# Kernel optimization log

Measured on AMD Instinct MI355X. Metric: run time of the kernel, lower is better.

Reference implementation:

```python
import jax, jax.numpy as jnp
import numpy as np


def _lstm_step(x, h, c, Wih, Whh, bih, bhh):
    # torch.nn.LSTMCell gate order: i, f, g, o
    g = x @ Wih.T + h @ Whh.T + bih + bhh
    i, f, gg, o = jnp.split(g, 4, axis=-1)
    c2 = jax.nn.sigmoid(f) * c + jax.nn.sigmoid(i) * jnp.tanh(gg)
    h2 = jax.nn.sigmoid(o) * jnp.tanh(c2)
    return h2, c2


def _run_dir(x_pad, mask, h0, c0, Wih, Whh, bih, bhh, reverse):
    # Masked scan == VariableRecurrent: rows past batch_sizes[t] keep frozen state.
    def step(carry, inp):
        h, c = carry
        x_t, m = inp
        h2, c2 = _lstm_step(x_t, h, c, Wih, Whh, bih, bhh)
        m = m[:, None]
        h = jnp.where(m, h2, h)
        c = jnp.where(m, c2, c)
        return (h, c), h
    (hT, cT), outs = jax.lax.scan(step, (h0, c0), (x_pad, mask), reverse=reverse)
    return hT, cT, outs


def setup_inputs():
    key = jax.random.key(0)
    B, T, D, CELL, L = 64, 1024, 256, 128, 2
    G = 4 * CELL  # 512
    lengths = np.array([T - 8 * b for b in range(B)])  # 1024 .. 520, descending
    batch_sizes = jnp.asarray([(lengths > t).sum() for t in range(T)], dtype=jnp.int32)
    total = int(lengths.sum())  # 49408
    ks = jax.random.split(key, 5)
    inp = jax.random.normal(ks[0], (total, D), dtype=jnp.float32)
    W_ih = jax.random.normal(ks[1], (2 * L, G, D), jnp.float32) * 0.05
    W_hh = jax.random.normal(ks[2], (2 * L, G, CELL), jnp.float32) * 0.05
    b_ih = jax.random.normal(ks[3], (2 * L, G), jnp.float32) * 0.05
    b_hh = jax.random.normal(ks[4], (2 * L, G), jnp.float32) * 0.05
    h0 = jnp.zeros((2 * L, B, CELL), jnp.float32)
    c0 = jnp.zeros((2 * L, B, CELL), jnp.float32)
    return {"input": inp, "batch_sizes": batch_sizes, "h0": h0, "c0": c0,
            "W_ih": W_ih, "W_hh": W_hh, "b_ih": b_ih, "b_hh": b_hh}


def reference(input, batch_sizes, h0, c0, W_ih, W_hh, b_ih, b_hh):
    T = batch_sizes.shape[0]
    B = h0.shape[1]
    total = input.shape[0]
    num_layers = W_ih.shape[0] // 2
    # packed <-> padded index math (static shapes; values from batch_sizes)
    offsets = jnp.concatenate([jnp.zeros((1,), batch_sizes.dtype),
                               jnp.cumsum(batch_sizes)[:-1]])  # [T]
    bidx = jnp.arange(B)
    mask = bidx[None, :] < batch_sizes[:, None]  # [T, B] valid rows per step
    gather_idx = jnp.clip(offsets[:, None] + bidx[None, :], 0, total - 1)
    x = input[gather_idx]  # padded [T, B, D]; invalid rows masked in scan
    tok = jnp.arange(total)
    t_idx = jnp.searchsorted(offsets, tok, side='right') - 1
    b_idx = tok - offsets[t_idx]
    hs, cs = [], []
    for l in range(num_layers):
        outs = []
        for d in range(2):  # layer ordering: fwd_l, rev_l (matches StackedRNN)
            k = 2 * l + d
            hT, cT, o = _run_dir(x, mask, h0[k], c0[k],
                                 W_ih[k], W_hh[k], b_ih[k], b_hh[k],
                                 reverse=(d == 1))
            hs.append(hT)
            cs.append(cT)
            outs.append(o)
        x = jnp.concatenate(outs, axis=-1)  # [T, B, hidden_size]
    h_n = jnp.stack(hs, 0)  # [total_layers, B, CELL]
    c_n = jnp.stack(cs, 0)
    packed_out = x[t_idx, b_idx]  # [total, hidden_size]
    return packed_out, h_n, c_n
```

## Files before the change

### kernel.cpp

```cpp
#include <hip/hip_runtime.h>
#include <hip/hip_fp16.h>
#include <hip/hip_bf16.h>


#define CELL 128
#define GATES 512
#define DIN 256
#define NB 64

typedef float f4_t __attribute__((ext_vector_type(4)));
typedef short bf8_t __attribute__((ext_vector_type(8)));
typedef _Float16 h2_t __attribute__((ext_vector_type(2)));

static __device__ __forceinline__ unsigned short f32_bf16(float f) {
  union { float f; unsigned int u; } v; v.f = f;
  unsigned int u = v.u;
  return (unsigned short)((u + 0x7fffu + ((u >> 16) & 1u)) >> 16);
}

__global__ void k_setup(const int* __restrict__ bs, int T,
                        int* __restrict__ offsets, int* __restrict__ lengths) {
  __shared__ int sbs[1024];
  int t = threadIdx.x;
  sbs[t] = (t < T) ? bs[t] : 0;
  __syncthreads();
  int sum = 0;
  for (int i = 0; i < t; ++i) sum += sbs[i];
  if (t < T) offsets[t] = sum;
  if (t < NB) {
    int c = 0;
    for (int i = 0; i < T; ++i) c += (sbs[i] > t) ? 1 : 0;
    lengths[t] = c;
  }
}

__global__ void k_convert(const float* __restrict__ x, unsigned short* __restrict__ xb, int nx,
                          const float* __restrict__ wih, unsigned short* __restrict__ wb, int nw,
                          const float* __restrict__ bih, const float* __restrict__ bhh,
                          float* __restrict__ bsum, int nb2) {
  int stride = gridDim.x * blockDim.x;
  int i0 = blockIdx.x * blockDim.x + threadIdx.x;
  for (int i = i0; i < nx; i += stride) xb[i] = f32_bf16(x[i]);
  for (int i = i0; i < nw; i += stride) wb[i] = f32_bf16(wih[i]);
  for (int i = i0; i < nb2; i += stride) bsum[i] = bih[i] + bhh[i];
}

__global__ __launch_bounds__(256) void k_gemm(
    const unsigned short* __restrict__ A,
    const unsigned short* __restrict__ W,
    const float* __restrict__ bsum,
    __half* __restrict__ C,
    int M, int lbase) {
  __shared__ __align__(16) unsigned short As[128 * 64];
  __shared__ __align__(16) unsigned short Bs[128 * 64];
  const int tid = threadIdx.x;
  const int lane = tid & 63;
  const int wave = tid >> 6;
  const int wm = wave >> 1, wn = wave & 1;
  const int m0 = blockIdx.x * 128;
  const int n0 = blockIdx.y * 128;

  f4_t acc[4][4];
#pragma unroll
  for (int i = 0; i < 4; ++i)
#pragma unroll
    for (int j = 0; j < 4; ++j) acc[i][j] = (f4_t){0.f, 0.f, 0.f, 0.f};

  for (int kt = 0; kt < 256; kt += 64) {
#pragma unroll
    for (int it = 0; it < 4; ++it) {
      int idx = it * 256 + tid;
      int row = idx >> 3;
      int gslot = (idx & 7) ^ (row & 7);
      int grow = m0 + row; if (grow > M - 1) grow = M - 1;
      __builtin_amdgcn_global_load_lds(
          (const __attribute__((address_space(1))) unsigned int*)(A + (size_t)grow * 256 + kt + gslot * 8),
          (__attribute__((address_space(3))) unsigned int*)(As + idx * 8), 16, 0, 0);
    }
#pragma unroll
    for (int it = 0; it < 4; ++it) {
      int idx = it * 256 + tid;
      int row = idx >> 3;
      int gslot = (idx & 7) ^ (row & 7);
      __builtin_amdgcn_global_load_lds(
          (const __attribute__((address_space(1))) unsigned int*)(W + (size_t)(lbase + n0 + row) * 256 + kt + gslot * 8),
          (__attribute__((address_space(3))) unsigned int*)(Bs + idx * 8), 16, 0, 0);
    }
    asm volatile("s_waitcnt vmcnt(0)" ::: "memory");
    __syncthreads();
#pragma unroll
    for (int kk = 0; kk < 2; ++kk) {
      bf8_t af[4], bfv[4];
#pragma unroll
      for (int i = 0; i < 4; ++i) {
        int arow = wm * 64 + i * 16 + (lane & 15);
        int aslot = (kk * 4 + (lane >> 4)) ^ (arow & 7);
        af[i] = *(const bf8_t*)(As + arow * 64 + aslot * 8);
        int brow = wn * 64 + i * 16 + (lane & 15);
        int bslot = (kk * 4 + (lane >> 4)) ^ (brow & 7);
        bfv[i] = *(const bf8_t*)(Bs + brow * 64 + bslot * 8);
      }
#pragma unroll
      for (int i = 0; i < 4; ++i)
#pragma unroll
        for (int j = 0; j < 4; ++j)
          acc[i][j] = __builtin_amdgcn_mfma_f32_16x16x32_bf16(af[i], bfv[j], acc[i][j], 0, 0, 0);
    }
    __syncthreads();
  }
#pragma unroll
  for (int i = 0; i < 4; ++i) {
#pragma unroll
    for (int j = 0; j < 4; ++j) {
      int col = n0 + wn * 64 + j * 16 + (lane & 15);
      float bv = bsum[lbase + col];
#pragma unroll
      for (int r = 0; r < 4; ++r) {
        int row = m0 + wm * 64 + i * 16 + (lane >> 4) * 4 + r;
        if (row < M) C[(size_t)row * 1024 + col] = (__half)(acc[i][j][r] + bv);
      }
    }
  }
}

#if defined(__has_builtin)
#if __has_builtin(__builtin_amdgcn_fdot2)
#define HAVE_FDOT2 1
#endif
#endif

static __device__ __forceinline__ float fdot2(h2_t a, h2_t b, float c) {
#ifdef HAVE_FDOT2
  return __builtin_amdgcn_fdot2(a, b, c, false);
#else
  return c + (float)a[0] * (float)b[0] + (float)a[1] * (float)b[1];
#endif
}
static __device__ __forceinline__ float sigm(float x) { return 1.f / (1.f + __expf(-x)); }
static __device__ __forceinline__ float tanh_(float x) { return 1.f - 2.f / (1.f + __expf(2.f * x)); }

static __device__ __forceinline__ float red16(float v) {
  return v + __int_as_float(__builtin_amdgcn_ds_swizzle(__float_as_int(v), 0x401F));
}
static __device__ __forceinline__ float red32(float v) {
  return v + __shfl_xor(v, 32, 64);
}

template <int LAYER>
__global__ __launch_bounds__(512) void k_rec(
    const __half* __restrict__ gates,
    const int* __restrict__ offsets,
    const int* __restrict__ lengths,
    const float* __restrict__ h0,
    const float* __restrict__ c0,
    const float* __restrict__ Whh,
    unsigned short* __restrict__ y1,
    float* __restrict__ outp,
    float* __restrict__ hn, float* __restrict__ cn,
    int T) {
  const int b = blockIdx.x >> 1;
  const int d = blockIdx.x & 1;
  const int k = 2 * LAYER + d;
  const int tid = threadIdx.x;
  const int lane = tid & 63;
  const int wave = tid >> 6;
  const int q = wave * 16 + (lane & 15);
  const int s = lane >> 4;
  const int L = lengths[b];

  __shared__ __align__(16) __half hb[2][CELL];
  __shared__ int toks[1024];

  for (int t = tid; t < T; t += 512) toks[t] = offsets[t] + b;

  h2_t wp[4][16];
  {
    const float* Wb = Whh + (size_t)k * GATES * CELL;
#pragma unroll
    for (int gi = 0; gi < 4; ++gi) {
      const float2* rowp = (const float2*)(Wb + (size_t)(gi * CELL + q) * CELL + s * 32);
#pragma unroll
      for (int j = 0; j < 16; ++j) {
        float2 w = rowp[j];
        h2_t p; p[0] = (_Float16)w.x; p[1] = (_Float16)w.y;
        wp[gi][j] = p;
      }
    }
  }

  float hcur = h0[(size_t)k * NB * CELL + b * CELL + q];
  float ccur = c0[(size_t)k * NB * CELL + b * CELL + q];
  if (s == 0) hb[0][q] = (__half)hcur;
  __syncthreads();

  __half gx0 = __half(0.f), gx1 = __half(0.f), gx2 = __half(0.f), gx3 = __half(0.f);
  int tokc = 0;
  if (L > 0) {
    tokc = toks[d ? (L - 1) : 0];
    const __half* gp = gates + (size_t)tokc * 1024 + d * GATES + q;
    gx0 = gp[0]; gx1 = gp[CELL]; gx2 = gp[2 * CELL]; gx3 = gp[3 * CELL];
  }

  int p = 0;
  for (int n = 0; n < L; ++n) {
    int tokn = tokc;
    if (n + 1 < L) tokn = toks[d ? (L - 2 - n) : (n + 1)];
    __half gn0, gn1, gn2, gn3;
    {
      const __half* gp = gates + (size_t)tokn * 1024 + d * GATES + q;
      gn0 = gp[0]; gn1 = gp[CELL]; gn2 = gp[2 * CELL]; gn3 = gp[3 * CELL];
    }

    const h2_t* hsh = (const h2_t*)hb[p];
    h2_t hp[16];
#pragma unroll
    for (int j = 0; j < 16; ++j) hp[j] = hsh[s * 16 + j];
    float a0 = 0.f, a1 = 0.f, a2 = 0.f, a3 = 0.f;
#pragma unroll
    for (int j = 0; j < 16; ++j) {
      a0 = fdot2(wp[0][j], hp[j], a0);
      a1 = fdot2(wp[1][j], hp[j], a1);
      a2 = fdot2(wp[2][j], hp[j], a2);
      a3 = fdot2(wp[3][j], hp[j], a3);
    }
    a0 = red32(red16(a0));
    a1 = red32(red16(a1));
    a2 = red32(red16(a2));
    a3 = red32(red16(a3));

    float gi = a0 + __half2float(gx0);
    float gf = a1 + __half2float(gx1);
    float gg = a2 + __half2float(gx2);
    float go = a3 + __half2float(gx3);
    float fi = sigm(gi), ff = sigm(gf), fg = tanh_(gg), fo = sigm(go);
    ccur = ff * ccur + fi * fg;
    hcur = fo * tanh_(ccur);

    if (s == 0) {
      hb[p ^ 1][q] = (__half)hcur;
      if (LAYER == 0)
        y1[(size_t)tokc * 256 + d * CELL + q] = f32_bf16(hcur);
      else
        outp[(size_t)tokc * 256 + d * CELL + q] = hcur;
    }
    __syncthreads();
    p ^= 1;
    gx0 = gn0; gx1 = gn1; gx2 = gn2; gx3 = gn3;
    tokc = tokn;
  }
  if (s == 0) {
    hn[(size_t)k * NB * CELL + b * CELL + q] = hcur;
    cn[(size_t)k * NB * CELL + b * CELL + q] = ccur;
  }
}

extern "C" void kernel_launch(void* const* d_in, const int* in_sizes, int n_in,
                              void* d_out, int out_size, void* d_ws, size_t ws_size,
                              hipStream_t stream) {
  const float* x   = (const float*)d_in[0];
  const int*   bs  = (const int*)d_in[1];
  const float* h0  = (const float*)d_in[2];
  const float* c0  = (const float*)d_in[3];
  const float* wih = (const float*)d_in[4];
  const float* whh = (const float*)d_in[5];
  const float* bih = (const float*)d_in[6];
  const float* bhh = (const float*)d_in[7];
  const int TOTAL = in_sizes[0] / DIN;
  const int T = in_sizes[1];

  char* ws = (char*)d_ws;
  size_t off = 0;
  auto alloc = [&](size_t bytes) {
    void* p = ws + off;
    off = (off + bytes + 255) & ~(size_t)255;
    return p;
  };
  int* offsets        = (int*)alloc((size_t)T * 4);
  int* lengths        = (int*)alloc(NB * 4);
  float* bsum         = (float*)alloc(2048 * 4);
  unsigned short* wb  = (unsigned short*)alloc((size_t)2048 * 256 * 2);
  unsigned short* xb  = (unsigned short*)alloc((size_t)TOTAL * 256 * 2);
  unsigned short* y1  = (unsigned short*)alloc((size_t)TOTAL * 256 * 2);
  __half* gates       = (__half*)alloc((size_t)TOTAL * 1024 * 2);

  float* outp = (float*)d_out;
  float* hn = outp + (size_t)TOTAL * 256;
  float* cn = hn + 4 * NB * CELL;

  k_setup<<<1, 1024, 0, stream>>>(bs, T, offsets, lengths);
  k_convert<<<1024, 256, 0, stream>>>(x, xb, TOTAL * 256,
                                      wih, wb, 4 * GATES * DIN,
                                      bih, bhh, bsum, 2048);
  dim3 ggrid((TOTAL + 127) / 128, 8);
  k_gemm<<<ggrid, 256, 0, stream>>>(xb, wb, bsum, gates, TOTAL, 0);
  k_rec<0><<<NB * 2, 512, 0, stream>>>(gates, offsets, lengths, h0, c0, whh,
                                       y1, nullptr, hn, cn, T);
  k_gemm<<<ggrid, 256, 0, stream>>>(y1, wb, bsum, gates, TOTAL, 1024);
  k_rec<1><<<NB * 2, 512, 0, stream>>>(gates, offsets, lengths, h0, c0, whh,
                                       nullptr, outp, hn, cn, T);
}
```

Before: 1.946 ms.

## Interleave gate columns and halve recurrent block threads with two-step prefetch

```diff
diff --git a/kernel.cpp b/kernel.cpp
--- a/kernel.cpp
+++ b/kernel.cpp
@@ -114,10 +114,12 @@
     for (int j = 0; j < 4; ++j) {
       int col = n0 + wn * 64 + j * 16 + (lane & 15);
       float bv = bsum[lbase + col];
+      int d_ = col >> 9, gate_ = (col >> 7) & 3, q_ = col & 127;
+      int ncol = d_ * 512 + q_ * 4 + gate_;
 #pragma unroll
       for (int r = 0; r < 4; ++r) {
         int row = m0 + wm * 64 + i * 16 + (lane >> 4) * 4 + r;
-        if (row < M) C[(size_t)row * 1024 + col] = (__half)(acc[i][j][r] + bv);
+        if (row < M) C[(size_t)row * 1024 + ncol] = (__half)(acc[i][j][r] + bv);
       }
     }
   }
@@ -139,15 +141,8 @@
 static __device__ __forceinline__ float sigm(float x) { return 1.f / (1.f + __expf(-x)); }
 static __device__ __forceinline__ float tanh_(float x) { return 1.f - 2.f / (1.f + __expf(2.f * x)); }
 
-static __device__ __forceinline__ float red16(float v) {
-  return v + __int_as_float(__builtin_amdgcn_ds_swizzle(__float_as_int(v), 0x401F));
-}
-static __device__ __forceinline__ float red32(float v) {
-  return v + __shfl_xor(v, 32, 64);
-}
-
 template <int LAYER>
-__global__ __launch_bounds__(512) void k_rec(
+__global__ __launch_bounds__(256) void k_rec(
     const __half* __restrict__ gates,
     const int* __restrict__ offsets,
     const int* __restrict__ lengths,
@@ -164,26 +159,26 @@
   const int tid = threadIdx.x;
   const int lane = tid & 63;
   const int wave = tid >> 6;
-  const int q = wave * 16 + (lane & 15);
-  const int s = lane >> 4;
+  const int q = wave * 32 + (lane & 31);
+  const int s = lane >> 5;
   const int L = lengths[b];
 
   __shared__ __align__(16) __half hb[2][CELL];
   __shared__ int toks[1024];
 
-  for (int t = tid; t < T; t += 512) toks[t] = offsets[t] + b;
-
-  h2_t wp[4][16];
+  for (int t = tid; t < T; t += 256) toks[t] = offsets[t] + b;
+
+  h2_t wp[4][32];
   {
     const float* Wb = Whh + (size_t)k * GATES * CELL;
 #pragma unroll
     for (int gi = 0; gi < 4; ++gi) {
-      const float2* rowp = (const float2*)(Wb + (size_t)(gi * CELL + q) * CELL + s * 32);
-#pragma unroll
-      for (int j = 0; j < 16; ++j) {
+      const float2* rowp = (const float2*)(Wb + (size_t)(gi * CELL + q) * CELL + s * 64);
+#pragma unroll
+      for (int j = 0; j < 32; ++j) {
         float2 w = rowp[j];
-        h2_t p; p[0] = (_Float16)w.x; p[1] = (_Float16)w.y;
-        wp[gi][j] = p;
+        h2_t pr; pr[0] = (_Float16)w.x; pr[1] = (_Float16)w.y;
+        wp[gi][j] = pr;
       }
     }
   }
@@ -193,49 +188,44 @@
   if (s == 0) hb[0][q] = (__half)hcur;
   __syncthreads();
 
-  __half gx0 = __half(0.f), gx1 = __half(0.f), gx2 = __half(0.f), gx3 = __half(0.f);
-  int tokc = 0;
-  if (L > 0) {
-    tokc = toks[d ? (L - 1) : 0];
-    const __half* gp = gates + (size_t)tokc * 1024 + d * GATES + q;
-    gx0 = gp[0]; gx1 = gp[CELL]; gx2 = gp[2 * CELL]; gx3 = gp[3 * CELL];
-  }
+  const __half* gbase = gates + (size_t)d * 512 + (size_t)q * 4;
+  auto tok_at = [&](int m) { int mm = (m < L) ? m : (L - 1); return toks[d ? (L - 1 - mm) : mm]; };
+  auto gload = [&](int m) { return *(const uint2*)(gbase + (size_t)tok_at(m) * 1024); };
+
+  uint2 gA = (L > 0) ? gload(0) : make_uint2(0, 0);
+  uint2 gB = (L > 1) ? gload(1) : gA;
 
   int p = 0;
-  for (int n = 0; n < L; ++n) {
-    int tokn = tokc;
-    if (n + 1 < L) tokn = toks[d ? (L - 2 - n) : (n + 1)];
-    __half gn0, gn1, gn2, gn3;
-    {
-      const __half* gp = gates + (size_t)tokn * 1024 + d * GATES + q;
-      gn0 = gp[0]; gn1 = gp[CELL]; gn2 = gp[2 * CELL]; gn3 = gp[3 * CELL];
-    }
-
-    const h2_t* hsh = (const h2_t*)hb[p];
-    h2_t hp[16];
-#pragma unroll
-    for (int j = 0; j < 16; ++j) hp[j] = hsh[s * 16 + j];
-    float a0 = 0.f, a1 = 0.f, a2 = 0.f, a3 = 0.f;
+  auto body = [&](int n, uint2& gcur) {
+    const h2_t* hsh = (const h2_t*)(&hb[p][0]) + s * 32;
+    h2_t hp[32];
+#pragma unroll
+    for (int j = 0; j < 32; ++j) hp[j] = hsh[j];
+    float x00 = 0.f, x01 = 0.f, x10 = 0.f, x11 = 0.f;
+    float x20 = 0.f, x21 = 0.f, x30 = 0.f, x31 = 0.f;
 #pragma unroll
     for (int j = 0; j < 16; ++j) {
-      a0 = fdot2(wp[0][j], hp[j], a0);
-      a1 = fdot2(wp[1][j], hp[j], a1);
-      a2 = fdot2(wp[2][j], hp[j], a2);
-      a3 = fdot2(wp[3][j], hp[j], a3);
-    }
-    a0 = red32(red16(a0));
-    a1 = red32(red16(a1));
-    a2 = red32(red16(a2));
-    a3 = red32(red16(a3));
-
-    float gi = a0 + __half2float(gx0);
-    float gf = a1 + __half2float(gx1);
-    float gg = a2 + __half2float(gx2);
-    float go = a3 + __half2float(gx3);
-    float fi = sigm(gi), ff = sigm(gf), fg = tanh_(gg), fo = sigm(go);
+      x00 = fdot2(wp[0][j], hp[j], x00); x01 = fdot2(wp[0][j + 16], hp[j + 16], x01);
+      x10 = fdot2(wp[1][j], hp[j], x10); x11 = fdot2(wp[1][j + 16], hp[j + 16], x11);
+      x20 = fdot2(wp[2][j], hp[j], x20); x21 = fdot2(wp[2][j + 16], hp[j + 16], x21);
+      x30 = fdot2(wp[3][j], hp[j], x30); x31 = fdot2(wp[3][j + 16], hp[j + 16], x31);
+    }
+    float f0 = x00 + x01, f1 = x10 + x11, f2 = x20 + x21, f3 = x30 + x31;
+    f0 += __shfl_xor(f0, 32, 64);
+    f1 += __shfl_xor(f1, 32, 64);
+    f2 += __shfl_xor(f2, 32, 64);
+    f3 += __shfl_xor(f3, 32, 64);
+
+    union { uint2 u; __half h[4]; } gg; gg.u = gcur;
+    float vi = f0 + (float)gg.h[0];
+    float vf = f1 + (float)gg.h[1];
+    float vg = f2 + (float)gg.h[2];
+    float vo = f3 + (float)gg.h[3];
+    float fi = sigm(vi), ff = sigm(vf), fg = tanh_(vg), fo = sigm(vo);
     ccur = ff * ccur + fi * fg;
     hcur = fo * tanh_(ccur);
 
+    int tokc = tok_at(n);
     if (s == 0) {
       hb[p ^ 1][q] = (__half)hcur;
       if (LAYER == 0)
@@ -243,11 +233,15 @@
       else
         outp[(size_t)tokc * 256 + d * CELL + q] = hcur;
     }
+    gcur = gload(n + 2);
     __syncthreads();
     p ^= 1;
-    gx0 = gn0; gx1 = gn1; gx2 = gn2; gx3 = gn3;
-    tokc = tokn;
-  }
+  };
+
+  int n = 0;
+  while (n + 1 < L) { body(n, gA); body(n + 1, gB); n += 2; }
+  if (n < L) body(n, gA);
+
   if (s == 0) {
     hn[(size_t)k * NB * CELL + b * CELL + q] = hcur;
     cn[(size_t)k * NB * CELL + b * CELL + q] = ccur;
@@ -293,9 +287,9 @@
                                       bih, bhh, bsum, 2048);
   dim3 ggrid((TOTAL + 127) / 128, 8);
   k_gemm<<<ggrid, 256, 0, stream>>>(xb, wb, bsum, gates, TOTAL, 0);
-  k_rec<0><<<NB * 2, 512, 0, stream>>>(gates, offsets, lengths, h0, c0, whh,
+  k_rec<0><<<NB * 2, 256, 0, stream>>>(gates, offsets, lengths, h0, c0, whh,
                                        y1, nullptr, hn, cn, T);
   k_gemm<<<ggrid, 256, 0, stream>>>(y1, wb, bsum, gates, TOTAL, 1024);
-  k_rec<1><<<NB * 2, 512, 0, stream>>>(gates, offsets, lengths, h0, c0, whh,
+  k_rec<1><<<NB * 2, 256, 0, stream>>>(gates, offsets, lengths, h0, c0, whh,
                                        nullptr, outp, hn, cn, T);
 }
```

New measurement: 1.912 ms. Within noise of the previous version (-1.8%).
